# Optimization experiments

Hardware: AMD Instinct MI355X
Metric: run time of the kernel (lower is better)

## Reference

```python
import jax, jax.numpy as jnp
import numpy as np

L, H, C = 2, 8, 128          # layers, heads, hidden_channels
D = C // H                   # head dim
NPAT, NICD, NNDC = 50000, 591, 2042
OUT = 90
E = 250000                   # edges per relation
# edge relations as (src_type, dst_type); node types: 0=patient, 1=icd, 2=ndc
ETYPES = [(0, 1), (1, 0), (0, 2), (2, 0)]


def _seg_softmax(logits, seg, n):
    # softmax over edges grouped by destination node (PyG `softmax`)
    m = jax.ops.segment_max(logits, seg, num_segments=n)
    e = jnp.exp(logits - m[seg])
    s = jax.ops.segment_sum(e, seg, num_segments=n)
    return e / s[seg]


def setup_inputs() -> dict:
    key = jax.random.key(0)
    ks = jax.random.split(key, 24)
    s = 1.0 / np.sqrt(C)
    n = lambda k, shape, sc: jax.random.normal(k, shape, dtype=jnp.float32) * sc
    return {
        "x_patient": n(ks[0], (NPAT, C), 1.0),
        "w_in_patient": n(ks[1], (C, C), s),
        "b_in_patient": jnp.zeros((C,), jnp.float32),
        "emb_icd": n(ks[2], (NICD, C), 0.1),
        "emb_ndc": n(ks[3], (NNDC, C), 0.1),
        "kw": n(ks[4], (L, 3, C, C), s), "kb": jnp.zeros((L, 3, C), jnp.float32),
        "qw": n(ks[5], (L, 3, C, C), s), "qb": jnp.zeros((L, 3, C), jnp.float32),
        "vw": n(ks[6], (L, 3, C, C), s), "vb": jnp.zeros((L, 3, C), jnp.float32),
        "aw": n(ks[7], (L, 3, C, C), s), "ab": jnp.zeros((L, 3, C), jnp.float32),
        "skip": jnp.ones((L, 3), jnp.float32),
        "a_rel": n(ks[8], (L, 4, H, D, D), 1.0 / np.sqrt(D)),
        "m_rel": n(ks[9], (L, 4, H, D, D), 1.0 / np.sqrt(D)),
        "p_rel": jnp.ones((L, 4, H), jnp.float32),
        "w_out": n(ks[10], (C, OUT), s),
        "b_out": jnp.zeros((OUT,), jnp.float32),
        "x_icd": jnp.arange(NICD, dtype=jnp.int32),
        "x_ndc": jnp.arange(NNDC, dtype=jnp.int32),
        "src_pi": jax.random.randint(ks[11], (E,), 0, NPAT, dtype=jnp.int32),
        "dst_pi": jax.random.randint(ks[12], (E,), 0, NICD, dtype=jnp.int32),
        "src_ip": jax.random.randint(ks[13], (E,), 0, NICD, dtype=jnp.int32),
        "dst_ip": jax.random.randint(ks[14], (E,), 0, NPAT, dtype=jnp.int32),
        "src_pn": jax.random.randint(ks[15], (E,), 0, NPAT, dtype=jnp.int32),
        "dst_pn": jax.random.randint(ks[16], (E,), 0, NNDC, dtype=jnp.int32),
        "src_np": jax.random.randint(ks[17], (E,), 0, NNDC, dtype=jnp.int32),
        "dst_np": jax.random.randint(ks[18], (E,), 0, NPAT, dtype=jnp.int32),
    }


def reference(x_patient, w_in_patient, b_in_patient, emb_icd, emb_ndc,
              kw, kb, qw, qb, vw, vb, aw, ab, skip,
              a_rel, m_rel, p_rel, w_out, b_out,
              x_icd, x_ndc,
              src_pi, dst_pi, src_ip, dst_ip, src_pn, dst_pn, src_np, dst_np):
    edges = [(src_pi, dst_pi), (src_ip, dst_ip), (src_pn, dst_pn), (src_np, dst_np)]
    sizes = [NPAT, NICD, NNDC]
    # per-type input projection / embedding + relu
    x = [jax.nn.relu(x_patient @ w_in_patient + b_in_patient),
         jax.nn.relu(emb_icd[x_icd]),
         jax.nn.relu(emb_ndc[x_ndc])]
    scale = 1.0 / np.sqrt(D)
    for l in range(L):
        k = [(x[t] @ kw[l, t] + kb[l, t]).reshape(-1, H, D) for t in range(3)]
        q = [(x[t] @ qw[l, t] + qb[l, t]).reshape(-1, H, D) for t in range(3)]
        v = [(x[t] @ vw[l, t] + vb[l, t]).reshape(-1, H, D) for t in range(3)]
        agg = [jnp.zeros((sizes[t], H, D), x[0].dtype) for t in range(3)]
        for r, (st, dt) in enumerate(ETYPES):
            src, dst = edges[r]
            kr = jnp.einsum('nhd,hde->nhe', k[st], a_rel[l, r])  # relation key transform
            vr = jnp.einsum('nhd,hde->nhe', v[st], m_rel[l, r])  # relation msg transform
            alpha = jnp.sum(q[dt][dst] * kr[src], axis=-1) * p_rel[l, r] * scale  # [E,H]
            alpha = _seg_softmax(alpha, dst, sizes[dt])
            agg[dt] = agg[dt] + jax.ops.segment_sum(vr[src] * alpha[:, :, None], dst, num_segments=sizes[dt])
        new_x = []
        for t in range(3):
            o = jax.nn.gelu(agg[t].reshape(-1, C)) @ aw[l, t] + ab[l, t]
            a = jax.nn.sigmoid(skip[l, t])
            new_x.append(a * o + (1.0 - a) * x[t])  # learned skip (dims match)
        x = new_x
    return jax.nn.sigmoid(x[0] @ w_out + b_out)
```

## Files before the change

### kernel.cpp

```cpp
#include <hip/hip_runtime.h>
#include <math.h>

#define CDIM  128
#define NHEAD 8
#define DHEAD 16
#define NPAT  50000
#define NICD  591
#define NNDC  2042
#define OUTN  90
#define NEDGE 250000
#define NLAYER 2
#define ALC   640

#define OFF0  0
#define OFF1  (NICD)
#define OFF2  (NICD + NPAT)
#define OFF3  (NICD + NPAT + NNDC)
#define NTOT  (NICD + NPAT + NNDC + NPAT)

#define LDP 40
#define CTILE 72
#define LOG2E 1.4426950408889634f

#define NSEG  (2 * NNDC)
#define NAGG  ((NPAT + 3) / 4)

typedef __attribute__((ext_vector_type(8))) short bf16x8;
typedef __attribute__((ext_vector_type(4))) float f32x4;

__device__ __forceinline__ float gelu_tanh(float x) {
    float x3 = x * x * x;
    return 0.5f * x * (1.0f + tanhf(0.7978845608028654f * (x + 0.044715f * x3)));
}
__device__ __forceinline__ float b2f(unsigned short u) {
    union { unsigned int i; float f; } v; v.i = ((unsigned int)u) << 16; return v.f;
}
__device__ __forceinline__ unsigned short f2b(float f) {
    union { float ff; unsigned int i; } v; v.ff = f;
    unsigned int i = v.i;
    return (unsigned short)((i + 0x7FFFu + ((i >> 16) & 1u)) >> 16);
}
__device__ __forceinline__ float2 b2x2(unsigned int u) {
    union { unsigned int i; float f; } lo, hi;
    lo.i = u << 16; hi.i = u & 0xFFFF0000u;
    return make_float2(lo.f, hi.f);
}

// ... 196 lines not shown
        #pragma unroll
        for (int tn = 0; tn < 2; tn++)
        #pragma unroll
        for (int r = 0; r < 4; r++) {
            int row = bm + wr * 32 + tm * 16 + quad * 4 + r;
            int col = bn + wc * 32 + tn * 16 + lm;
            if (row >= M || col >= N) continue;
            float v = acc[tm][tn][r] + (bias ? bias[col] : 0.f);
            if (act == 1) v = fmaxf(v, 0.f);
            else if (act == 2) v = 1.0f / (1.0f + expf(-v));
            ((float*)Cp)[(size_t)row * ldc + col] = v;
        }
    }
}

__global__ __launch_bounds__(256) void wprep_all(
    const float* __restrict__ qw, const float* __restrict__ aw,
    const float* __restrict__ w_in, const float* __restrict__ w_out,
    unsigned short* __restrict__ Wb0, unsigned short* __restrict__ Wb1,
    unsigned short* __restrict__ Wb2, unsigned short* __restrict__ Wtaw,
    unsigned short* __restrict__ Wtin, unsigned short* __restrict__ Wtout)
{
    __shared__ float tile[32][33];
    int z = blockIdx.z;
    const float* s; unsigned short* d; int N = 128;
    if (z < 2)       { s = qw + (size_t)z * 3 * 16384;              d = Wb0 + (size_t)z * 640 * 128; }
    else if (z < 4)  { s = qw + 16384 + (size_t)(z - 2) * 3 * 16384; d = Wb1 + (size_t)(z - 2) * 384 * 128; }
    else if (z < 6)  { s = qw + 2 * 16384 + (size_t)(z - 4) * 3 * 16384; d = Wb2 + (size_t)(z - 4) * 384 * 128; }
    else if (z < 12) { s = aw + (size_t)(z - 6) * 16384;            d = Wtaw + (size_t)(z - 6) * 16384; }
    else if (z == 12){ s = w_in;  d = Wtin; }
    else             { s = w_out; d = Wtout; N = OUTN; }
    int k0 = blockIdx.x * 32, n0 = blockIdx.y * 32;
    int tx = threadIdx.x & 31, ty = threadIdx.x >> 5;
    for (int i = 0; i < 32; i += 8) {
        int k = k0 + ty + i, n = n0 + tx;
        tile[ty + i][tx] = (k < 128 && n < N) ? s[(size_t)k * N + n] : 0.f;
    }
    __syncthreads();
    for (int i = 0; i < 32; i += 8) {
        int n = n0 + ty + i, k = k0 + tx;
        if (n < N && k < 128) d[(size_t)n * 128 + k] = f2b(tile[tx][ty + i]);
    }
}

__global__ __launch_bounds__(256) void wcomp_kernel(
    const float* __restrict__ kw, const float* __restrict__ vw,
    const float* __restrict__ a_rel, const float* __restrict__ m_rel,
    const float* __restrict__ kb, const float* __restrict__ vb,
    unsigned short* __restrict__ Wb0, unsigned short* __restrict__ Wb1,
    unsigned short* __restrict__ Wb2,
    float* __restrict__ bb0, float* __restrict__ bb1, float* __restrict__ bb2)
{
    int s = blockIdx.x;
    int l = s >> 3, j = s & 7;
    int t, isV, r, rowoff, nw;
    unsigned short* Wb; float* bb;
    switch (j) {
      case 0: t=0; isV=0; r=0; Wb=Wb0; bb=bb0; rowoff=128; nw=640; break;
      case 1: t=0; isV=1; r=0; Wb=Wb0; bb=bb0; rowoff=256; nw=640; break;
      case 2: t=0; isV=0; r=2; Wb=Wb0; bb=bb0; rowoff=384; nw=640; break;
      case 3: t=0; isV=1; r=2; Wb=Wb0; bb=bb0; rowoff=512; nw=640; break;
      case 4: t=1; isV=0; r=1; Wb=Wb1; bb=bb1; rowoff=128; nw=384; break;
      case 5: t=1; isV=1; r=1; Wb=Wb1; bb=bb1; rowoff=256; nw=384; break;
      case 6: t=2; isV=0; r=3; Wb=Wb2; bb=bb2; rowoff=128; nw=384; break;
      default:t=2; isV=1; r=3; Wb=Wb2; bb=bb2; rowoff=256; nw=384; break;
    }
    const float* W = (isV ? vw : kw) + (size_t)(l * 3 + t) * 16384;
    const float* A = (isV ? m_rel : a_rel) + (size_t)(l * 4 + r) * 2048;
    const float* B = (isV ? vb : kb) + (size_t)(l * 3 + t) * 128;
    unsigned short* dst = Wb + (size_t)l * nw * 128 + (size_t)rowoff * 128;
    float* bdst = bb + (size_t)l * nw + rowoff;
    int n = threadIdx.x & 127;
    int kh = threadIdx.x >> 7;
    int h = n >> 4, e = n & 15;
    float Ar[16];
    #pragma unroll
    for (int d = 0; d < 16; d++) Ar[d] = A[h * 256 + d * 16 + e];
    for (int k = kh * 64; k < kh * 64 + 64; k++) {
        float acc = 0.f;
        const float* wr = W + (size_t)k * 128 + h * 16;
        #pragma unroll
        for (int d = 0; d < 16; d++) acc += wr[d] * Ar[d];
        dst[(size_t)n * 128 + k] = f2b(acc);
    }
    if (kh == 0) {
        float acc = 0.f;
        const float* br = B + h * 16;
        #pragma unroll
        for (int d = 0; d < 16; d++) acc += br[d] * Ar[d];
        bdst[n] = acc;
    }
}

__global__ void biasq_kernel(const float* __restrict__ qb,
                             float* __restrict__ bb0, float* __restrict__ bb1,
                             float* __restrict__ bb2) {
    int t = blockIdx.x * blockDim.x + threadIdx.x;
    if (t >= 6 * 128) return;
    int g = t >> 7, c = t & 127;
    int l = g / 3, ty = g % 3;
    float v = qb[g * 128 + c];
    if (ty == 0) bb0[l * 640 + c] = v;
    else if (ty == 1) bb1[l * 384 + c] = v;
    else bb2[l * 384 + c] = v;
}

__global__ __launch_bounds__(256) void hist4_kernel(
    const int* __restrict__ d0, const int* __restrict__ d1,
    const int* __restrict__ d2, const int* __restrict__ d3,
    int* __restrict__ deg)
{
    __shared__ int lh[2048];
    int rel = blockIdx.y;
    int t = threadIdx.x;
    const int* dp = (rel == 0) ? d0 : (rel == 1) ? d1 : (rel == 2) ? d2 : d3;
    int off = (rel == 0) ? OFF0 : (rel == 1) ? OFF1 : (rel == 2) ? OFF2 : OFF3;
    if (rel == 1 || rel == 3) {
        for (int e = blockIdx.x * 256 + t; e < NEDGE; e += gridDim.x * 256)
            atomicAdd(&deg[off + dp[e]], 1);
// ... 18 lines not shown
    int b = blockIdx.x, t = threadIdx.x;
    int base = b * 1024 + t * 4;
    int s = 0;
    if (base + 3 < n) {
        int4 v = *(const int4*)(deg + base);
        s = v.x + v.y + v.z + v.w;
    } else {
        for (int i = 0; i < 4; i++) if (base + i < n) s += deg[base + i];
    }
    red[t] = s;
    __syncthreads();
    for (int o = 128; o; o >>= 1) { if (t < o) red[t] += red[t + o]; __syncthreads(); }
    if (t == 0) part[b] = red[0];
}

__global__ __launch_bounds__(128) void scanB_kernel(int* __restrict__ part, int nb)
{
    __shared__ int s[256];
    int t = threadIdx.x;
    for (int i = t; i < nb; i += 128) s[i] = part[i];
    __syncthreads();
    if (t == 0) { int run = 0; for (int i = 0; i < nb; i++) { int v = s[i]; s[i] = run; run += v; } }
    __syncthreads();
    for (int i = t; i < nb; i += 128) part[i] = s[i];
}

__global__ __launch_bounds__(256) void scanC_kernel(
    const int* __restrict__ deg, const int* __restrict__ part,
    int* __restrict__ rp0, int* __restrict__ rp1,
    int* __restrict__ rp2, int* __restrict__ rp3,
    int* __restrict__ cursor, int n)
{
    __shared__ int red[256];
    int b = blockIdx.x, t = threadIdx.x;
    int base = b * 1024 + t * 4;
    int v[4] = {0, 0, 0, 0};
    if (base + 3 < n) {
        int4 q = *(const int4*)(deg + base);
        v[0] = q.x; v[1] = q.y; v[2] = q.z; v[3] = q.w;
    } else {
        for (int i = 0; i < 4; i++) if (base + i < n) v[i] = deg[base + i];
    }
    red[t] = v[0] + v[1] + v[2] + v[3];
    __syncthreads();
    for (int off = 1; off < 256; off <<= 1) {
        int y = (t >= off) ? red[t - off] : 0;
        __syncthreads();
        red[t] += y;
        __syncthreads();
    }
    int run = part[b] + ((t == 0) ? 0 : red[t - 1]);
    for (int i = 0; i < 4; i++) {
        int g = base + i;
        if (g < n) {
            cursor[g] = run;
            int r, loc;
            if      (g < OFF1) { r = 0; loc = g; }
            else if (g < OFF2) { r = 1; loc = g - OFF1; }
            else if (g < OFF3) { r = 2; loc = g - OFF2; }
            else               { r = 3; loc = g - OFF3; }
            int Sl = run - r * NEDGE;
            ((r == 0) ? rp0 : (r == 1) ? rp1 : (r == 2) ? rp2 : rp3)[loc] = Sl;
            run += v[i];
        }
    }
    if (b == 0 && t == 0) {
        rp0[NICD] = NEDGE; rp1[NPAT] = NEDGE; rp2[NNDC] = NEDGE; rp3[NPAT] = NEDGE;
    }
}

__global__ __launch_bounds__(256) void scatter_pack_kernel(
    const int* __restrict__ s0, const int* __restrict__ d0,
    const int* __restrict__ s1, const int* __restrict__ d1,
    const int* __restrict__ s2, const int* __restrict__ d2,
    const int* __restrict__ s3, const int* __restrict__ d3,
    int* __restrict__ cursor, unsigned int* __restrict__ es)
{
    __shared__ int lcnt[2048];
    __shared__ int lbase[2048];
    int rel = blockIdx.y;
    int t = threadIdx.x;
    const int* sp = (rel == 0) ? s0 : (rel == 1) ? s1 : (rel == 2) ? s2 : s3;
    const int* dp = (rel == 0) ? d0 : (rel == 1) ? d1 : (rel == 2) ? d2 : d3;
    int off = (rel == 0) ? OFF0 : (rel == 1) ? OFF1 : (rel == 2) ? OFF2 : OFF3;
    if (rel == 1 || rel == 3) {
        for (int e = blockIdx.x * 256 + t; e < NEDGE; e += gridDim.x * 256) {
            int d = dp[e];
            int p = atomicAdd(&cursor[off + d], 1);
            es[p] = ((unsigned int)sp[e] << 16) | (unsigned int)d;
        }
    } else {
        int nb = (rel == 0) ? NICD : NNDC;
        int per = (NEDGE + gridDim.x - 1) / gridDim.x;
        int e0 = blockIdx.x * per, e1 = min(e0 + per, NEDGE);
        for (int i = t; i < nb; i += 256) lcnt[i] = 0;
        __syncthreads();
        for (int e = e0 + t; e < e1; e += 256) atomicAdd(&lcnt[dp[e]], 1);
        __syncthreads();
        for (int i = t; i < nb; i += 256) {
            int c = lcnt[i];
            lbase[i] = c ? atomicAdd(&cursor[off + i], c) : 0;
            lcnt[i] = 0;
        }
        __syncthreads();
        for (int e = e0 + t; e < e1; e += 256) {
            int d = dp[e];
            int p = lbase[d] + atomicAdd(&lcnt[d], 1);
            es[p] = ((unsigned int)sp[e] << 16) | (unsigned int)d;
        }
    }
}

__global__ void gather_relu2_kernel(
    const float* __restrict__ embA, const int* __restrict__ idxA,
    unsigned short* __restrict__ outA, int nA,
    const float* __restrict__ embB, const int* __restrict__ idxB,
    unsigned short* __restrict__ outB, int nB)
{
    int t = blockIdx.x * blockDim.x + threadIdx.x;
    int totA = nA * CDIM;
    if (t < totA) {
        int r = t >> 7, c = t & 127;
        outA[t] = f2b(fmaxf(embA[(size_t)idxA[r] * CDIM + c], 0.f));
    } else if (t < totA + nB * CDIM) {
        int u = t - totA;
        int r = u >> 7, c = u & 127;
        outB[u] = f2b(fmaxf(embB[(size_t)idxB[r] * CDIM + c], 0.f));
    }
}

__device__ __forceinline__ float dot16_bf(const unsigned short* a,
                                          const unsigned short* b) {
    const uint4* ap = (const uint4*)a;
    const uint4* bp = (const uint4*)b;
    uint4 a0 = ap[0], a1 = ap[1], b0 = bp[0], b1 = bp[1];
    unsigned int au[8] = {a0.x, a0.y, a0.z, a0.w, a1.x, a1.y, a1.z, a1.w};
    unsigned int bu[8] = {b0.x, b0.y, b0.z, b0.w, b1.x, b1.y, b1.z, b1.w};
    float acc = 0.f;
    #pragma unroll
    for (int j = 0; j < 8; j++) {
        float2 x = b2x2(au[j]), y = b2x2(bu[j]);
        acc += x.x * y.x + x.y * y.y;
// ... 134 lines not shown
        for (; i < deg; i += 4) {
            int e0 = sl[i];
            unsigned int u0 = *(const unsigned int*)(vr + (size_t)e0 * ldsrc + 2 * l);
            float w0 = wl[i * NHEAD + hh];
            float2 v0 = b2x2(u0);
            acc0 += w0 * v0.x;
            acc1 += w0 * v0.y;
        }
        p3f[g][l][0] = acc0;
        p3f[g][l][1] = acc1;
        __syncthreads();
        if (t < 128) {
            int c = t;
            float v = p3f[0][c >> 1][c & 1] + p3f[1][c >> 1][c & 1]
                    + p3f[2][c >> 1][c & 1] + p3f[3][c >> 1][c & 1];
            agg[(size_t)n * CDIM + c] = f2b(gelu_tanh(v * sinv[c >> 4]));
        }
    } else {
        float* p3 = (float*)p3f;
        float mx = -1e30f;
        for (int i = j; i < deg; i += 32) {
            int sn = es[r0 + i] >> 16;
            float a = dot16_q(qa, qb, kr + (size_t)sn * ldsrc + h * DHEAD) * ph;
            alpha[(size_t)(r0 + i) * NHEAD + h] = a;
            mx = fmaxf(mx, a);
        }
        mx = fmaxf(mx, __shfl_xor(mx, 8));
        mx = fmaxf(mx, __shfl_xor(mx, 16));
        mx = fmaxf(mx, __shfl_xor(mx, 32));
        if (lane < 8) wred[wv][h] = mx;
        __syncthreads();
// ... 30 lines not shown
            float w2 = alpha[(size_t)(r0 + i + 4) * NHEAD + (c >> 4)];
            float w3 = alpha[(size_t)(r0 + i + 6) * NHEAD + (c >> 4)];
            float v0 = b2f(vr[(size_t)(e0 >> 16) * ldsrc + c]);
            float v1 = b2f(vr[(size_t)(e1 >> 16) * ldsrc + c]);
            float v2 = b2f(vr[(size_t)(e2 >> 16) * ldsrc + c]);
            float v3 = b2f(vr[(size_t)(e3 >> 16) * ldsrc + c]);
            acc += w0 * v0 + w1 * v1 + w2 * v2 + w3 * v3;
        }
        for (; i < deg; i += 2) {
            unsigned int e0 = es[r0 + i];
            float w0 = alpha[(size_t)(r0 + i) * NHEAD + (c >> 4)];
            acc += w0 * b2f(vr[(size_t)(e0 >> 16) * ldsrc + c]);
        }
        p3[t] = acc * hsi;
        __syncthreads();
        if (half == 0) agg[(size_t)n * CDIM + c] = f2b(gelu_tanh(p3[c] + p3[128 + c]));
    }
}

__global__ __launch_bounds__(256) void agg2_kernel(
    const int* __restrict__ rp1, const unsigned int* __restrict__ es1,
    const int* __restrict__ rp3, const unsigned int* __restrict__ es3,
    const unsigned short* __restrict__ q, int ldq,
    const unsigned short* __restrict__ kr1, const unsigned short* __restrict__ vr1, int ld1,
    const unsigned short* __restrict__ kr3, const unsigned short* __restrict__ vr3, int ld3,
    const float* __restrict__ prel1, const float* __restrict__ prel3,
    unsigned short* __restrict__ agg, int nd)
{
    __shared__ float wls[4][128 * NHEAD];
    __shared__ int slo[4][128];
    int wv  = threadIdx.x >> 6;
    int wid = (blockIdx.x * 256 + threadIdx.x) >> 6;
    int lane = threadIdx.x & 63;
    if (wid >= nd) return;
    float* wl = wls[wv];
    int* sl = slo[wv];
    int h = lane & 7, j = lane >> 3;
    int hc = lane >> 3;
    const unsigned short* qbase = q + (size_t)wid * ldq;
    float acc0 = 0.f, acc1 = 0.f;

    int r0a = rp1[wid], degA = rp1[wid + 1] - r0a;
    int r0b = rp3[wid], degB = rp3[wid + 1] - r0b;

    if (degA <= 64 && degB <= 64) {
        const unsigned short* qrow = qbase + h * DHEAD;
        float phA = prel1[h] * 0.25f * LOG2E;
        float phB = prel3[h] * 0.25f * LOG2E;
        int dOfs = (int)(kr3 - kr1);
        float mA = -1e30f, mB = -1e30f;
        for (int i = j; i < degA; i += 8) {
            int sn = es1[r0a + i] >> 16;
            int off = sn * ld1;
            float a = dot16_bf(qrow, kr1 + off + h * DHEAD) * phA;
            wl[i * NHEAD + h] = a;
            if (h == 0) sl[i] = off;
            mA = fmaxf(mA, a);
        }
        for (int i = j; i < degB; i += 8) {
            int sn = es3[r0b + i] >> 16;
            int off = sn * ld3;
            float a = dot16_bf(qrow, kr3 + off + h * DHEAD) * phB;
            wl[(degA + i) * NHEAD + h] = a;
            if (h == 0) sl[degA + i] = dOfs + off;
            mB = fmaxf(mB, a);
        }
        mA = fmaxf(mA, __shfl_xor(mA, 8));   mB = fmaxf(mB, __shfl_xor(mB, 8));
        mA = fmaxf(mA, __shfl_xor(mA, 16));  mB = fmaxf(mB, __shfl_xor(mB, 16));
        mA = fmaxf(mA, __shfl_xor(mA, 32));  mB = fmaxf(mB, __shfl_xor(mB, 32));

        int dtot = degA + degB;
        float sA = 0.f, sB = 0.f;
        for (int i = j; i < dtot; i += 8) {
            bool isA = i < degA;
            float e = exp2f(wl[i * NHEAD + h] - (isA ? mA : mB));
            wl[i * NHEAD + h] = e;
            sA += isA ? e : 0.f;
            sB += isA ? 0.f : e;
        }
        sA += __shfl_xor(sA, 8);   sB += __shfl_xor(sB, 8);
        sA += __shfl_xor(sA, 16);  sB += __shfl_xor(sB, 16);
        sA += __shfl_xor(sA, 32);  sB += __shfl_xor(sB, 32);
        float siA = (sA > 0.f) ? 1.0f / sA : 0.f;
        float siB = (sB > 0.f) ? 1.0f / sB : 0.f;
        for (int i = j; i < dtot; i += 8)
            wl[i * NHEAD + h] *= (i < degA) ? siA : siB;

        int i = 0;
        for (; i + 4 <= dtot; i += 4) {
            int o0 = sl[i + 0], o1 = sl[i + 1], o2 = sl[i + 2], o3 = sl[i + 3];
            unsigned int u0 = *(const unsigned int*)(vr1 + o0 + 2 * lane);
            unsigned int u1 = *(const unsigned int*)(vr1 + o1 + 2 * lane);
            unsigned int u2 = *(const unsigned int*)(vr1 + o2 + 2 * lane);
            unsigned int u3 = *(const unsigned int*)(vr1 + o3 + 2 * lane);
            float w0 = wl[(i + 0) * NHEAD + hc];
            float w1 = wl[(i + 1) * NHEAD + hc];
            float w2 = wl[(i + 2) * NHEAD + hc];
            float w3 = wl[(i + 3) * NHEAD + hc];
            float2 v0 = b2x2(u0), v1 = b2x2(u1), v2 = b2x2(u2), v3 = b2x2(u3);
            acc0 += w0 * v0.x + w1 * v1.x + w2 * v2.x + w3 * v3.x;
            acc1 += w0 * v0.y + w1 * v1.y + w2 * v2.y + w3 * v3.y;
        }
        for (; i < dtot; i++) {
            int o0 = sl[i];
            unsigned int u0 = *(const unsigned int*)(vr1 + o0 + 2 * lane);
            float w0 = wl[i * NHEAD + hc];
            float2 v0 = b2x2(u0);
            acc0 += w0 * v0.x; acc1 += w0 * v0.y;
        }
    } else {
        #pragma unroll
        for (int rr = 0; rr < 2; rr++) {
            const unsigned int* es = rr ? es3 : es1;
            const unsigned short* kr = rr ? kr3 : kr1;
            const unsigned short* vr = rr ? vr3 : vr1;
            int ld = rr ? ld3 : ld1;
            const float* prel = rr ? prel3 : prel1;
            int r0 = rr ? r0b : r0a;
            int deg = rr ? degB : degA;
            if (deg <= 0) continue;
            const unsigned short* qrow = qbase + h * DHEAD;
            float ph = prel[h] * 0.25f * LOG2E;
            bool small = (deg <= 64);

            float m = -1e30f;
// ... 32 lines not shown
            const unsigned short* qrow_hc = qbase + hc * DHEAD;
            for (int i = 0; i < deg; i++) {
                unsigned int sv = es[r0 + i] >> 16;
                unsigned int pv = *(const unsigned int*)(vr + (size_t)sv * ld + 2 * lane);
                float2 v = b2x2(pv);
                float wgt;
                if (small) wgt = wl[i * NHEAD + hc];
                else {
                    float a = dot16_bf(qrow_hc, kr + (size_t)sv * ld + hc * DHEAD) * ph_hc;
                    wgt = exp2f(a - m_hc) * si_hc;
                }
                acc0 += wgt * v.x;
                acc1 += wgt * v.y;
            }
        }
    }
    unsigned int packed = (unsigned int)f2b(gelu_tanh(acc0))
                        | ((unsigned int)f2b(gelu_tanh(acc1)) << 16);
    *(unsigned int*)(agg + (size_t)wid * CDIM + 2 * lane) = packed;
}

extern "C" void kernel_launch(void* const* d_in, const int* in_sizes, int n_in,
                              void* d_out, int out_size, void* d_ws, size_t ws_size,
                              hipStream_t stream)
{
    const float* x_patient = (const float*)d_in[0];
    const float* w_in      = (const float*)d_in[1];
    const float* b_in      = (const float*)d_in[2];
    const float* emb_icd   = (const float*)d_in[3];
    const float* emb_ndc   = (const float*)d_in[4];
    const float* kw        = (const float*)d_in[5];
    const float* kbias     = (const float*)d_in[6];
    const float* qw        = (const float*)d_in[7];
// ... 45 lines not shown
    int* deg    = (int*)alloc((size_t)NTOT * 4);
    int* cursor = (int*)alloc((size_t)NTOT * 4);
    int* part   = (int*)alloc((size_t)256 * 4);
    unsigned short* Wb0   = (unsigned short*)alloc((size_t)2 * 640 * 128 * 2);
    unsigned short* Wb1   = (unsigned short*)alloc((size_t)2 * 384 * 128 * 2);
    unsigned short* Wb2   = (unsigned short*)alloc((size_t)2 * 384 * 128 * 2);
    unsigned short* Wtaw  = (unsigned short*)alloc((size_t)6 * 128 * 128 * 2);
    unsigned short* Wtin  = (unsigned short*)alloc((size_t)128 * 128 * 2);
    unsigned short* Wtout = (unsigned short*)alloc((size_t)OUTN * 128 * 2);
    float* bb0 = (float*)alloc((size_t)2 * 640 * 4);
    float* bb1 = (float*)alloc((size_t)2 * 384 * 4);
    float* bb2 = (float*)alloc((size_t)2 * 384 * 4);
    unsigned int* esRel[4];
    for (int r = 0; r < 4; r++) esRel[r] = esbig + (size_t)r * NEDGE;

    wprep_all<<<dim3(4, 4, 14), 256, 0, stream>>>(qw, aw, w_in, w_out,
        Wb0, Wb1, Wb2, Wtaw, Wtin, Wtout);
    wcomp_kernel<<<16, 256, 0, stream>>>(kw, vw, a_rel, m_rel, kbias, vbias,
        Wb0, Wb1, Wb2, bb0, bb1, bb2);
    biasq_kernel<<<3, 256, 0, stream>>>(qbias, bb0, bb1, bb2);

    {
        const int NB = (NTOT + 1023) / 1024;
        hipMemsetAsync(deg, 0, (size_t)NTOT * 4, stream);
        hist4_kernel<<<dim3(64, 4), 256, 0, stream>>>(
            edst[0], edst[1], edst[2], edst[3], deg);
        scanA_kernel<<<NB, 256, 0, stream>>>(deg, part, NTOT);
        scanB_kernel<<<1, 128, 0, stream>>>(part, NB);
        scanC_kernel<<<NB, 256, 0, stream>>>(deg, part,
            rowptr[0], rowptr[1], rowptr[2], rowptr[3], cursor, NTOT);
        scatter_pack_kernel<<<dim3(64, 4), 256, 0, stream>>>(
            esrc[0], edst[0], esrc[1], edst[1], esrc[2], edst[2], esrc[3], edst[3],
            cursor, esbig);
    }

    {
        int ntile = 2;
        int nwg = ((NPAT + 63) / 64) * ntile;
        gemm_xs<<<dim3(nwg), dim3(256), 0, stream>>>(x_patient, 1, 128, Wtin, b_in,
            xb[0], 0, 128, NPAT, 128, 1, ntile, nullptr, 0, nullptr, 0);
    }
    gather_relu2_kernel<<<((NICD + NNDC) * CDIM + 255) / 256, 256, 0, stream>>>(
        emb_icd, x_icd, xb[1], NICD, emb_ndc, x_ndc, xb[2], NNDC);

    const int ntP0 = 640 / 64, nwgP0 = ((NPAT + 63) / 64) * ntP0;
    const int ntP1 = 384 / 64, nwgP1 = ((NICD + 63) / 64) * ntP1;
    const int ntP2 = 384 / 64, nwgP2 = ((NNDC + 63) / 64) * ntP2;
    const int ntS  = 128 / 64;
    const int nwgS0 = ((NPAT + 63) / 64) * ntS;
    const int nwgS1 = ((NICD + 63) / 64) * ntS;
    const int nwgS2 = ((NNDC + 63) / 64) * ntS;

    for (int l = 0; l < NLAYER; l++) {
        gemm3_kernel<<<dim3(nwgP0 + nwgP1 + nwgP2), dim3(256), 0, stream>>>(
            xb[0], Wb0 + (size_t)l * 640 * 128, bb0 + (size_t)l * 640, P0,
            NPAT, 640, ntP0, nwgP0,
            xb[1], Wb1 + (size_t)l * 384 * 128, bb1 + (size_t)l * 384, P1,
            NICD, 384, ntP1, nwgP0 + nwgP1,
// ... 34 lines not shown
```

Measured before the change: 512.4 us.

## Merge prep launches, fold scan phase, fuse scatter with input GEMM, faster GELU

```diff
diff --git a/kernel.cpp b/kernel.cpp
--- a/kernel.cpp
+++ b/kernel.cpp
@@ -17,6 +17,7 @@
 #define OFF2  (NICD + NPAT)
 #define OFF3  (NICD + NPAT + NNDC)
 #define NTOT  (NICD + NPAT + NNDC + NPAT)
+#define NB_SCAN ((NTOT + 1023) / 1024)
 
 #define LDP 40
 #define CTILE 72
@@ -25,12 +26,24 @@
 #define NSEG  (2 * NNDC)
 #define NAGG  ((NPAT + 3) / 4)
 
+#define PB_W  224
+#define PB_C  (PB_W + 16)
+#define PB_Q  (PB_C + 3)
+#define PB_Z  (PB_Q + NB_SCAN)
+#define PB_G  (PB_Z + (((NICD + NNDC) * CDIM + 255) / 256))
+
+#define SI_SCAT 256
+#define SI_NWG  (((NPAT + 63) / 64) * 2)
+
 typedef __attribute__((ext_vector_type(8))) short bf16x8;
 typedef __attribute__((ext_vector_type(4))) float f32x4;
 
-__device__ __forceinline__ float gelu_tanh(float x) {
+__device__ __forceinline__ float gelu_fast(float x) {
     float x3 = x * x * x;
-    return 0.5f * x * (1.0f + tanhf(0.7978845608028654f * (x + 0.044715f * x3)));
+    float y = 0.7978845608028654f * (x + 0.044715f * x3);
+    float e = exp2f(y * (2.0f * LOG2E));
+    float t = 1.0f - 2.0f * __builtin_amdgcn_rcpf(e + 1.0f);
+    return 0.5f * x * (1.0f + t);
 }
 __device__ __forceinline__ float b2f(unsigned short u) {
     union { unsigned int i; float f; } v; v.i = ((unsigned int)u) << 16; return v.f;
@@ -257,95 +270,113 @@
     }
 }
 
-__global__ __launch_bounds__(256) void wprep_all(
+__global__ __launch_bounds__(256) void prep_all_kernel(
     const float* __restrict__ qw, const float* __restrict__ aw,
     const float* __restrict__ w_in, const float* __restrict__ w_out,
     unsigned short* __restrict__ Wb0, unsigned short* __restrict__ Wb1,
     unsigned short* __restrict__ Wb2, unsigned short* __restrict__ Wtaw,
-    unsigned short* __restrict__ Wtin, unsigned short* __restrict__ Wtout)
-{
-    __shared__ float tile[32][33];
-    int z = blockIdx.z;
-    const float* s; unsigned short* d; int N = 128;
-    if (z < 2)       { s = qw + (size_t)z * 3 * 16384;              d = Wb0 + (size_t)z * 640 * 128; }
-    else if (z < 4)  { s = qw + 16384 + (size_t)(z - 2) * 3 * 16384; d = Wb1 + (size_t)(z - 2) * 384 * 128; }
-    else if (z < 6)  { s = qw + 2 * 16384 + (size_t)(z - 4) * 3 * 16384; d = Wb2 + (size_t)(z - 4) * 384 * 128; }
-    else if (z < 12) { s = aw + (size_t)(z - 6) * 16384;            d = Wtaw + (size_t)(z - 6) * 16384; }
-    else if (z == 12){ s = w_in;  d = Wtin; }
-    else             { s = w_out; d = Wtout; N = OUTN; }
-    int k0 = blockIdx.x * 32, n0 = blockIdx.y * 32;
-    int tx = threadIdx.x & 31, ty = threadIdx.x >> 5;
-    for (int i = 0; i < 32; i += 8) {
-        int k = k0 + ty + i, n = n0 + tx;
-        tile[ty + i][tx] = (k < 128 && n < N) ? s[(size_t)k * N + n] : 0.f;
-    }
-    __syncthreads();
-    for (int i = 0; i < 32; i += 8) {
-        int n = n0 + ty + i, k = k0 + tx;
-        if (n < N && k < 128) d[(size_t)n * 128 + k] = f2b(tile[tx][ty + i]);
-    }
-}
-
-__global__ __launch_bounds__(256) void wcomp_kernel(
+    unsigned short* __restrict__ Wtin, unsigned short* __restrict__ Wtout,
     const float* __restrict__ kw, const float* __restrict__ vw,
     const float* __restrict__ a_rel, const float* __restrict__ m_rel,
     const float* __restrict__ kb, const float* __restrict__ vb,
-    unsigned short* __restrict__ Wb0, unsigned short* __restrict__ Wb1,
-    unsigned short* __restrict__ Wb2,
-    float* __restrict__ bb0, float* __restrict__ bb1, float* __restrict__ bb2)
+    float* __restrict__ bb0, float* __restrict__ bb1, float* __restrict__ bb2,
+    const float* __restrict__ qb,
+    int* __restrict__ deg,
+    const float* __restrict__ emb_icd, const int* __restrict__ x_icd,
+    unsigned short* __restrict__ xb1,
+    const float* __restrict__ emb_ndc, const int* __restrict__ x_ndc,
+    unsigned short* __restrict__ xb2)
 {
-    int s = blockIdx.x;
-    int l = s >> 3, j = s & 7;
-    int t, isV, r, rowoff, nw;
-    unsigned short* Wb; float* bb;
-    switch (j) {
-      case 0: t=0; isV=0; r=0; Wb=Wb0; bb=bb0; rowoff=128; nw=640; break;
-      case 1: t=0; isV=1; r=0; Wb=Wb0; bb=bb0; rowoff=256; nw=640; break;
-      case 2: t=0; isV=0; r=2; Wb=Wb0; bb=bb0; rowoff=384; nw=640; break;
-      case 3: t=0; isV=1; r=2; Wb=Wb0; bb=bb0; rowoff=512; nw=640; break;
-      case 4: t=1; isV=0; r=1; Wb=Wb1; bb=bb1; rowoff=128; nw=384; break;
-      case 5: t=1; isV=1; r=1; Wb=Wb1; bb=bb1; rowoff=256; nw=384; break;
-      case 6: t=2; isV=0; r=3; Wb=Wb2; bb=bb2; rowoff=128; nw=384; break;
-      default:t=2; isV=1; r=3; Wb=Wb2; bb=bb2; rowoff=256; nw=384; break;
-    }
-    const float* W = (isV ? vw : kw) + (size_t)(l * 3 + t) * 16384;
-    const float* A = (isV ? m_rel : a_rel) + (size_t)(l * 4 + r) * 2048;
-    const float* B = (isV ? vb : kb) + (size_t)(l * 3 + t) * 128;
-    unsigned short* dst = Wb + (size_t)l * nw * 128 + (size_t)rowoff * 128;
-    float* bdst = bb + (size_t)l * nw + rowoff;
-    int n = threadIdx.x & 127;
-    int kh = threadIdx.x >> 7;
-    int h = n >> 4, e = n & 15;
-    float Ar[16];
-    #pragma unroll
-    for (int d = 0; d < 16; d++) Ar[d] = A[h * 256 + d * 16 + e];
-    for (int k = kh * 64; k < kh * 64 + 64; k++) {
-        float acc = 0.f;
-        const float* wr = W + (size_t)k * 128 + h * 16;
-        #pragma unroll
-        for (int d = 0; d < 16; d++) acc += wr[d] * Ar[d];
-        dst[(size_t)n * 128 + k] = f2b(acc);
-    }
-    if (kh == 0) {
-        float acc = 0.f;
-        const float* br = B + h * 16;
-        #pragma unroll
-        for (int d = 0; d < 16; d++) acc += br[d] * Ar[d];
-        bdst[n] = acc;
-    }
-}
-
-__global__ void biasq_kernel(const float* __restrict__ qb,
-                             float* __restrict__ bb0, float* __restrict__ bb1,
-                             float* __restrict__ bb2) {
-    int t = blockIdx.x * blockDim.x + threadIdx.x;
-    if (t >= 6 * 128) return;
-    int g = t >> 7, c = t & 127;
-    int l = g / 3, ty = g % 3;
-    float v = qb[g * 128 + c];
-    if (ty == 0) bb0[l * 640 + c] = v;
-    else if (ty == 1) bb1[l * 384 + c] = v;
-    else bb2[l * 384 + c] = v;
+    __shared__ float tile[32][33];
+    int b = blockIdx.x;
+    int tid = threadIdx.x;
+    if (b < PB_W) {
+        int z = b >> 4, rem = b & 15;
+        int by = rem >> 2, bx = rem & 3;
+        const float* s; unsigned short* d; int N = 128;
+        if (z < 2)       { s = qw + (size_t)z * 3 * 16384;               d = Wb0 + (size_t)z * 640 * 128; }
+        else if (z < 4)  { s = qw + 16384 + (size_t)(z - 2) * 3 * 16384; d = Wb1 + (size_t)(z - 2) * 384 * 128; }
+        else if (z < 6)  { s = qw + 2 * 16384 + (size_t)(z - 4) * 3 * 16384; d = Wb2 + (size_t)(z - 4) * 384 * 128; }
+        else if (z < 12) { s = aw + (size_t)(z - 6) * 16384;             d = Wtaw + (size_t)(z - 6) * 16384; }
+        else if (z == 12){ s = w_in;  d = Wtin; }
+        else             { s = w_out; d = Wtout; N = OUTN; }
+        int k0 = bx * 32, n0 = by * 32;
+        int tx = tid & 31, ty = tid >> 5;
+        for (int i = 0; i < 32; i += 8) {
+            int k = k0 + ty + i, n = n0 + tx;
+            tile[ty + i][tx] = (k < 128 && n < N) ? s[(size_t)k * N + n] : 0.f;
+        }
+        __syncthreads();
+        for (int i = 0; i < 32; i += 8) {
+            int n = n0 + ty + i, k = k0 + tx;
+            if (n < N && k < 128) d[(size_t)n * 128 + k] = f2b(tile[tx][ty + i]);
+        }
+    } else if (b < PB_C) {
+        int s = b - PB_W;
+        int l = s >> 3, j = s & 7;
+        int ty, isV, r, rowoff, nw;
+        unsigned short* Wb; float* bb;
+        switch (j) {
+          case 0: ty=0; isV=0; r=0; Wb=Wb0; bb=bb0; rowoff=128; nw=640; break;
+          case 1: ty=0; isV=1; r=0; Wb=Wb0; bb=bb0; rowoff=256; nw=640; break;
+          case 2: ty=0; isV=0; r=2; Wb=Wb0; bb=bb0; rowoff=384; nw=640; break;
+          case 3: ty=0; isV=1; r=2; Wb=Wb0; bb=bb0; rowoff=512; nw=640; break;
+          case 4: ty=1; isV=0; r=1; Wb=Wb1; bb=bb1; rowoff=128; nw=384; break;
+          case 5: ty=1; isV=1; r=1; Wb=Wb1; bb=bb1; rowoff=256; nw=384; break;
+          case 6: ty=2; isV=0; r=3; Wb=Wb2; bb=bb2; rowoff=128; nw=384; break;
+          default:ty=2; isV=1; r=3; Wb=Wb2; bb=bb2; rowoff=256; nw=384; break;
+        }
+        const float* W = (isV ? vw : kw) + (size_t)(l * 3 + ty) * 16384;
+        const float* A = (isV ? m_rel : a_rel) + (size_t)(l * 4 + r) * 2048;
+        const float* B = (isV ? vb : kb) + (size_t)(l * 3 + ty) * 128;
+        unsigned short* dst = Wb + (size_t)l * nw * 128 + (size_t)rowoff * 128;
+        float* bdst = bb + (size_t)l * nw + rowoff;
+        int n = tid & 127;
+        int kh = tid >> 7;
+        int h = n >> 4, e = n & 15;
+        float Ar[16];
+        #pragma unroll
+        for (int d = 0; d < 16; d++) Ar[d] = A[h * 256 + d * 16 + e];
+        for (int k = kh * 64; k < kh * 64 + 64; k++) {
+            float acc = 0.f;
+            const float* wr = W + (size_t)k * 128 + h * 16;
+            #pragma unroll
+            for (int d = 0; d < 16; d++) acc += wr[d] * Ar[d];
+            dst[(size_t)n * 128 + k] = f2b(acc);
+        }
+        if (kh == 0) {
+            float acc = 0.f;
+            const float* br = B + h * 16;
+            #pragma unroll
+            for (int d = 0; d < 16; d++) acc += br[d] * Ar[d];
+            bdst[n] = acc;
+        }
+    } else if (b < PB_Q) {
+        int t = (b - PB_C) * 256 + tid;
+        if (t < 6 * 128) {
+            int g = t >> 7, c = t & 127;
+            int l = g / 3, ty = g % 3;
+            float v = qb[g * 128 + c];
+            if (ty == 0) bb0[l * 640 + c] = v;
+            else if (ty == 1) bb1[l * 384 + c] = v;
+            else bb2[l * 384 + c] = v;
+        }
+    } else if (b < PB_Z) {
+        int base = (b - PB_Q) * 1024 + tid * 4;
+        if (base + 3 < NTOT) *(int4*)(deg + base) = make_int4(0, 0, 0, 0);
+        else for (int i = 0; i < 4; i++) if (base + i < NTOT) deg[base + i] = 0;
+    } else {
+        int t = (b - PB_Z) * 256 + tid;
+        int totA = NICD * CDIM;
+        if (t < totA) {
+            int r = t >> 7, c = t & 127;
+            xb1[t] = f2b(fmaxf(emb_icd[(size_t)x_icd[r] * CDIM + c], 0.f));
+        } else if (t < totA + NNDC * CDIM) {
+            int u = t - totA;
+            int r = u >> 7, c = u & 127;
+            xb2[u] = f2b(fmaxf(emb_ndc[(size_t)x_ndc[r] * CDIM + c], 0.f));
+        }
+    }
 }
 
 __global__ __launch_bounds__(256) void hist4_kernel(
@@ -394,25 +425,21 @@
     if (t == 0) part[b] = red[0];
 }
 
-__global__ __launch_bounds__(128) void scanB_kernel(int* __restrict__ part, int nb)
-{
-    __shared__ int s[256];
-    int t = threadIdx.x;
-    for (int i = t; i < nb; i += 128) s[i] = part[i];
-    __syncthreads();
-    if (t == 0) { int run = 0; for (int i = 0; i < nb; i++) { int v = s[i]; s[i] = run; run += v; } }
-    __syncthreads();
-    for (int i = t; i < nb; i += 128) part[i] = s[i];
-}
-
-__global__ __launch_bounds__(256) void scanC_kernel(
+__global__ __launch_bounds__(256) void scanC2_kernel(
     const int* __restrict__ deg, const int* __restrict__ part,
     int* __restrict__ rp0, int* __restrict__ rp1,
     int* __restrict__ rp2, int* __restrict__ rp3,
     int* __restrict__ cursor, int n)
 {
     __shared__ int red[256];
+    __shared__ int pre[128];
     int b = blockIdx.x, t = threadIdx.x;
+    if (t < 128) pre[t] = (t < b) ? part[t] : 0;
+    __syncthreads();
+    for (int o = 64; o; o >>= 1) { if (t < o) pre[t] += pre[t + o]; __syncthreads(); }
+    int pbase = pre[0];
+    __syncthreads();
+
     int base = b * 1024 + t * 4;
     int v[4] = {0, 0, 0, 0};
     if (base + 3 < n) {
@@ -429,7 +456,7 @@
         red[t] += y;
         __syncthreads();
     }
-    int run = part[b] + ((t == 0) ? 0 : red[t - 1]);
+    int run = pbase + ((t == 0) ? 0 : red[t - 1]);
     for (int i = 0; i < 4; i++) {
         int g = base + i;
         if (g < n) {
@@ -449,63 +476,120 @@
     }
 }
 
-__global__ __launch_bounds__(256) void scatter_pack_kernel(
+__global__ __launch_bounds__(256) void scat_in_kernel(
     const int* __restrict__ s0, const int* __restrict__ d0,
     const int* __restrict__ s1, const int* __restrict__ d1,
     const int* __restrict__ s2, const int* __restrict__ d2,
     const int* __restrict__ s3, const int* __restrict__ d3,
-    int* __restrict__ cursor, unsigned int* __restrict__ es)
+    int* __restrict__ cursor, unsigned int* __restrict__ es,
+    const float* __restrict__ Axp, const unsigned short* __restrict__ Wtin,
+    const float* __restrict__ b_in, unsigned short* __restrict__ xb0)
 {
-    __shared__ int lcnt[2048];
-    __shared__ int lbase[2048];
-    int rel = blockIdx.y;
+    __shared__ __align__(16) char smem[19456];
+    int b = blockIdx.x;
     int t = threadIdx.x;
-    const int* sp = (rel == 0) ? s0 : (rel == 1) ? s1 : (rel == 2) ? s2 : s3;
-    const int* dp = (rel == 0) ? d0 : (rel == 1) ? d1 : (rel == 2) ? d2 : d3;
-    int off = (rel == 0) ? OFF0 : (rel == 1) ? OFF1 : (rel == 2) ? OFF2 : OFF3;
-    if (rel == 1 || rel == 3) {
-        for (int e = blockIdx.x * 256 + t; e < NEDGE; e += gridDim.x * 256) {
-            int d = dp[e];
-            int p = atomicAdd(&cursor[off + d], 1);
-            es[p] = ((unsigned int)sp[e] << 16) | (unsigned int)d;
+    if (b < SI_SCAT) {
+        int* lcnt = (int*)smem;
+        int* lbase = lcnt + 2048;
+        int rel = b >> 6;
+        int bx = b & 63;
+        const int* sp = (rel == 0) ? s0 : (rel == 1) ? s1 : (rel == 2) ? s2 : s3;
+        const int* dp = (rel == 0) ? d0 : (rel == 1) ? d1 : (rel == 2) ? d2 : d3;
+        int off = (rel == 0) ? OFF0 : (rel == 1) ? OFF1 : (rel == 2) ? OFF2 : OFF3;
+        if (rel == 1 || rel == 3) {
+            for (int e = bx * 256 + t; e < NEDGE; e += 64 * 256) {
+                int d = dp[e];
+                int p = atomicAdd(&cursor[off + d], 1);
+                es[p] = ((unsigned int)sp[e] << 16) | (unsigned int)d;
+            }
+        } else {
+            int nb = (rel == 0) ? NICD : NNDC;
+            int per = (NEDGE + 63) / 64;
+            int e0 = bx * per, e1 = min(e0 + per, NEDGE);
+            for (int i = t; i < nb; i += 256) lcnt[i] = 0;
+            __syncthreads();
+            for (int e = e0 + t; e < e1; e += 256) atomicAdd(&lcnt[dp[e]], 1);
+            __syncthreads();
+            for (int i = t; i < nb; i += 256) {
+                int c = lcnt[i];
+                lbase[i] = c ? atomicAdd(&cursor[off + i], c) : 0;
+                lcnt[i] = 0;
+            }
+            __syncthreads();
+            for (int e = e0 + t; e < e1; e += 256) {
+                int d = dp[e];
+                int p = lbase[d] + atomicAdd(&lcnt[d], 1);
+                es[p] = ((unsigned int)sp[e] << 16) | (unsigned int)d;
+            }
         }
     } else {
-        int nb = (rel == 0) ? NICD : NNDC;
-        int per = (NEDGE + gridDim.x - 1) / gridDim.x;
-        int e0 = blockIdx.x * per, e1 = min(e0 + per, NEDGE);
-        for (int i = t; i < nb; i += 256) lcnt[i] = 0;
-        __syncthreads();
-        for (int e = e0 + t; e < e1; e += 256) atomicAdd(&lcnt[dp[e]], 1);
-        __syncthreads();
-        for (int i = t; i < nb; i += 256) {
-            int c = lcnt[i];
-            lbase[i] = c ? atomicAdd(&cursor[off + i], c) : 0;
-            lcnt[i] = 0;
-        }
-        __syncthreads();
-        for (int e = e0 + t; e < e1; e += 256) {
-            int d = dp[e];
-            int p = lbase[d] + atomicAdd(&lcnt[d], 1);
-            es[p] = ((unsigned int)sp[e] << 16) | (unsigned int)d;
-        }
-    }
-}
-
-__global__ void gather_relu2_kernel(
-    const float* __restrict__ embA, const int* __restrict__ idxA,
-    unsigned short* __restrict__ outA, int nA,
-    const float* __restrict__ embB, const int* __restrict__ idxB,
-    unsigned short* __restrict__ outB, int nB)
-{
-    int t = blockIdx.x * blockDim.x + threadIdx.x;
-    int totA = nA * CDIM;
-    if (t < totA) {
-        int r = t >> 7, c = t & 127;
-        outA[t] = f2b(fmaxf(embA[(size_t)idxA[r] * CDIM + c], 0.f));
-    } else if (t < totA + nB * CDIM) {
-        int u = t - totA;
-        int r = u >> 7, c = u & 127;
-        outB[u] = f2b(fmaxf(embB[(size_t)idxB[r] * CDIM + c], 0.f));
+        unsigned short* Al = (unsigned short*)smem;
+        unsigned short* Bl = Al + 64 * LDP;
+        unsigned short* Cst = Bl + 64 * LDP;
+        int u = b - SI_SCAT;
+        int nwg = SI_NWG;
+        int qq = nwg >> 3, rr = nwg & 7;
+        int xcd = u & 7, idx = u >> 3;
+        int wgid = (xcd < rr ? xcd * (qq + 1) : rr * (qq + 1) + (xcd - rr) * qq) + idx;
+        int bm = (wgid >> 1) * 64, bn = (wgid & 1) * 64;
+
+        int lane = t & 63, w = t >> 6;
+        int wr = w >> 1, wc = w & 1;
+        int quad = lane >> 4, lm = lane & 15;
+        f32x4 acc[2][2] = {};
+        const int srow = t >> 2;
+        const int skq  = (t & 3) * 8;
+
+        for (int k0 = 0; k0 < 128; k0 += 32) {
+            {
+                int row = bm + srow;
+                float f[8] = {0.f,0.f,0.f,0.f,0.f,0.f,0.f,0.f};
+                if (row < NPAT) {
+                    const float4* ap = (const float4*)(Axp + (size_t)row * 128 + k0 + skq);
+                    float4 u0 = ap[0], u1 = ap[1];
+                    f[0]=u0.x; f[1]=u0.y; f[2]=u0.z; f[3]=u0.w;
+                    f[4]=u1.x; f[5]=u1.y; f[6]=u1.z; f[7]=u1.w;
+                }
+                unsigned short v[8];
+                for (int i = 0; i < 8; i++) v[i] = f2b(f[i]);
+                *(uint4*)&Al[srow * LDP + skq] = *(uint4*)v;
+            }
+            {
+                int n = bn + srow;
+                *(uint4*)&Bl[srow * LDP + skq] = *(const uint4*)(Wtin + (size_t)n * 128 + k0 + skq);
+            }
+            __syncthreads();
+            bf16x8 af[2], bfr[2];
+            #pragma unroll
+            for (int i = 0; i < 2; i++) {
+                af[i]  = *(const bf16x8*)&Al[(wr * 32 + i * 16 + lm) * LDP + quad * 8];
+                bfr[i] = *(const bf16x8*)&Bl[(wc * 32 + i * 16 + lm) * LDP + quad * 8];
+            }
+            acc[0][0] = __builtin_amdgcn_mfma_f32_16x16x32_bf16(af[0], bfr[0], acc[0][0], 0, 0, 0);
+            acc[0][1] = __builtin_amdgcn_mfma_f32_16x16x32_bf16(af[0], bfr[1], acc[0][1], 0, 0, 0);
+            acc[1][0] = __builtin_amdgcn_mfma_f32_16x16x32_bf16(af[1], bfr[0], acc[1][0], 0, 0, 0);
+            acc[1][1] = __builtin_amdgcn_mfma_f32_16x16x32_bf16(af[1], bfr[1], acc[1][1], 0, 0, 0);
+            __syncthreads();
+        }
+        #pragma unroll
+        for (int tm = 0; tm < 2; tm++)
+        #pragma unroll
+        for (int tn = 0; tn < 2; tn++)
+        #pragma unroll
+        for (int r = 0; r < 4; r++) {
+            int lrow = wr * 32 + tm * 16 + quad * 4 + r;
+            int lcol = wc * 32 + tn * 16 + lm;
+            float v = acc[tm][tn][r] + b_in[bn + lcol];
+            v = fmaxf(v, 0.f);
+            Cst[lrow * CTILE + lcol] = f2b(v);
+        }
+        __syncthreads();
+        int row = t >> 2, seg = (t & 3) * 16;
+        if (bm + row < NPAT) {
+            unsigned short* dst = xb0 + (size_t)(bm + row) * 128 + bn + seg;
+            *(uint4*)dst       = *(const uint4*)&Cst[row * CTILE + seg];
+            *(uint4*)(dst + 8) = *(const uint4*)&Cst[row * CTILE + seg + 8];
+        }
     }
 }
 
@@ -670,7 +754,7 @@
             int c = t;
             float v = p3f[0][c >> 1][c & 1] + p3f[1][c >> 1][c & 1]
                     + p3f[2][c >> 1][c & 1] + p3f[3][c >> 1][c & 1];
-            agg[(size_t)n * CDIM + c] = f2b(gelu_tanh(v * sinv[c >> 4]));
+            agg[(size_t)n * CDIM + c] = f2b(gelu_fast(v * sinv[c >> 4]));
         }
     } else {
         float* p3 = (float*)p3f;
@@ -731,7 +815,7 @@
         }
         p3[t] = acc * hsi;
         __syncthreads();
-        if (half == 0) agg[(size_t)n * CDIM + c] = f2b(gelu_tanh(p3[c] + p3[128 + c]));
+        if (half == 0) agg[(size_t)n * CDIM + c] = f2b(gelu_fast(p3[c] + p3[128 + c]));
     }
 }
 
@@ -755,13 +839,14 @@
     int h = lane & 7, j = lane >> 3;
     int hc = lane >> 3;
     const unsigned short* qbase = q + (size_t)wid * ldq;
-    float acc0 = 0.f, acc1 = 0.f;
 
     int r0a = rp1[wid], degA = rp1[wid + 1] - r0a;
     int r0b = rp3[wid], degB = rp3[wid + 1] - r0b;
 
+    float o0, o1;
     if (degA <= 64 && degB <= 64) {
         const unsigned short* qrow = qbase + h * DHEAD;
+        uint4 qa = ((const uint4*)qrow)[0], qb = ((const uint4*)qrow)[1];
         float phA = prel1[h] * 0.25f * LOG2E;
         float phB = prel3[h] * 0.25f * LOG2E;
         int dOfs = (int)(kr3 - kr1);
@@ -769,7 +854,7 @@
         for (int i = j; i < degA; i += 8) {
             int sn = es1[r0a + i] >> 16;
             int off = sn * ld1;
-            float a = dot16_bf(qrow, kr1 + off + h * DHEAD) * phA;
+            float a = dot16_q(qa, qb, kr1 + off + h * DHEAD) * phA;
             wl[i * NHEAD + h] = a;
             if (h == 0) sl[i] = off;
             mA = fmaxf(mA, a);
@@ -777,7 +862,7 @@
         for (int i = j; i < degB; i += 8) {
             int sn = es3[r0b + i] >> 16;
             int off = sn * ld3;
-            float a = dot16_bf(qrow, kr3 + off + h * DHEAD) * phB;
+            float a = dot16_q(qa, qb, kr3 + off + h * DHEAD) * phB;
             wl[(degA + i) * NHEAD + h] = a;
             if (h == 0) sl[degA + i] = dOfs + off;
             mB = fmaxf(mB, a);
@@ -800,32 +885,57 @@
         sA += __shfl_xor(sA, 32);  sB += __shfl_xor(sB, 32);
         float siA = (sA > 0.f) ? 1.0f / sA : 0.f;
         float siB = (sB > 0.f) ? 1.0f / sB : 0.f;
-        for (int i = j; i < dtot; i += 8)
-            wl[i * NHEAD + h] *= (i < degA) ? siA : siB;
-
+        float siAh = __shfl(siA, hc);
+        float siBh = __shfl(siB, hc);
+
+        float accA0 = 0.f, accA1 = 0.f, accB0 = 0.f, accB1 = 0.f;
         int i = 0;
-        for (; i + 4 <= dtot; i += 4) {
-            int o0 = sl[i + 0], o1 = sl[i + 1], o2 = sl[i + 2], o3 = sl[i + 3];
-            unsigned int u0 = *(const unsigned int*)(vr1 + o0 + 2 * lane);
-            unsigned int u1 = *(const unsigned int*)(vr1 + o1 + 2 * lane);
-            unsigned int u2 = *(const unsigned int*)(vr1 + o2 + 2 * lane);
-            unsigned int u3 = *(const unsigned int*)(vr1 + o3 + 2 * lane);
+        for (; i + 4 <= degA; i += 4) {
+            int oo0 = sl[i + 0], oo1 = sl[i + 1], oo2 = sl[i + 2], oo3 = sl[i + 3];
+            unsigned int u0 = *(const unsigned int*)(vr1 + oo0 + 2 * lane);
+            unsigned int u1 = *(const unsigned int*)(vr1 + oo1 + 2 * lane);
+            unsigned int u2 = *(const unsigned int*)(vr1 + oo2 + 2 * lane);
+            unsigned int u3 = *(const unsigned int*)(vr1 + oo3 + 2 * lane);
             float w0 = wl[(i + 0) * NHEAD + hc];
             float w1 = wl[(i + 1) * NHEAD + hc];
             float w2 = wl[(i + 2) * NHEAD + hc];
             float w3 = wl[(i + 3) * NHEAD + hc];
             float2 v0 = b2x2(u0), v1 = b2x2(u1), v2 = b2x2(u2), v3 = b2x2(u3);
-            acc0 += w0 * v0.x + w1 * v1.x + w2 * v2.x + w3 * v3.x;
-            acc1 += w0 * v0.y + w1 * v1.y + w2 * v2.y + w3 * v3.y;
-        }
-        for (; i < dtot; i++) {
-            int o0 = sl[i];
-            unsigned int u0 = *(const unsigned int*)(vr1 + o0 + 2 * lane);
+            accA0 += w0 * v0.x + w1 * v1.x + w2 * v2.x + w3 * v3.x;
+            accA1 += w0 * v0.y + w1 * v1.y + w2 * v2.y + w3 * v3.y;
+        }
+        for (; i < degA; i++) {
+            int oo = sl[i];
+            unsigned int u0 = *(const unsigned int*)(vr1 + oo + 2 * lane);
             float w0 = wl[i * NHEAD + hc];
             float2 v0 = b2x2(u0);
-            acc0 += w0 * v0.x; acc1 += w0 * v0.y;
-        }
+            accA0 += w0 * v0.x; accA1 += w0 * v0.y;
+        }
+        for (; i + 4 <= dtot; i += 4) {
+            int oo0 = sl[i + 0], oo1 = sl[i + 1], oo2 = sl[i + 2], oo3 = sl[i + 3];
+            unsigned int u0 = *(const unsigned int*)(vr1 + oo0 + 2 * lane);
+            unsigned int u1 = *(const unsigned int*)(vr1 + oo1 + 2 * lane);
+            unsigned int u2 = *(const unsigned int*)(vr1 + oo2 + 2 * lane);
+            unsigned int u3 = *(const unsigned int*)(vr1 + oo3 + 2 * lane);
+            float w0 = wl[(i + 0) * NHEAD + hc];
+            float w1 = wl[(i + 1) * NHEAD + hc];
+            float w2 = wl[(i + 2) * NHEAD + hc];
+            float w3 = wl[(i + 3) * NHEAD + hc];
+            float2 v0 = b2x2(u0), v1 = b2x2(u1), v2 = b2x2(u2), v3 = b2x2(u3);
+            accB0 += w0 * v0.x + w1 * v1.x + w2 * v2.x + w3 * v3.x;
+            accB1 += w0 * v0.y + w1 * v1.y + w2 * v2.y + w3 * v3.y;
+        }
+        for (; i < dtot; i++) {
+            int oo = sl[i];
+            unsigned int u0 = *(const unsigned int*)(vr1 + oo + 2 * lane);
+            float w0 = wl[i * NHEAD + hc];
+            float2 v0 = b2x2(u0);
+            accB0 += w0 * v0.x; accB1 += w0 * v0.y;
+        }
+        o0 = accA0 * siAh + accB0 * siBh;
+        o1 = accA1 * siAh + accB1 * siBh;
     } else {
+        float acc0 = 0.f, acc1 = 0.f;
         #pragma unroll
         for (int rr = 0; rr < 2; rr++) {
             const unsigned int* es = rr ? es3 : es1;
@@ -888,9 +998,10 @@
                 acc1 += wgt * v.y;
             }
         }
-    }
-    unsigned int packed = (unsigned int)f2b(gelu_tanh(acc0))
-                        | ((unsigned int)f2b(gelu_tanh(acc1)) << 16);
+        o0 = acc0; o1 = acc1;
+    }
+    unsigned int packed = (unsigned int)f2b(gelu_fast(o0))
+                        | ((unsigned int)f2b(gelu_fast(o1)) << 16);
     *(unsigned int*)(agg + (size_t)wid * CDIM + 2 * lane) = packed;
 }
 
@@ -966,34 +1077,20 @@
     unsigned int* esRel[4];
     for (int r = 0; r < 4; r++) esRel[r] = esbig + (size_t)r * NEDGE;
 
-    wprep_all<<<dim3(4, 4, 14), 256, 0, stream>>>(qw, aw, w_in, w_out,
-        Wb0, Wb1, Wb2, Wtaw, Wtin, Wtout);
-    wcomp_kernel<<<16, 256, 0, stream>>>(kw, vw, a_rel, m_rel, kbias, vbias,
-        Wb0, Wb1, Wb2, bb0, bb1, bb2);
-    biasq_kernel<<<3, 256, 0, stream>>>(qbias, bb0, bb1, bb2);
-
-    {
-        const int NB = (NTOT + 1023) / 1024;
-        hipMemsetAsync(deg, 0, (size_t)NTOT * 4, stream);
-        hist4_kernel<<<dim3(64, 4), 256, 0, stream>>>(
-            edst[0], edst[1], edst[2], edst[3], deg);
-        scanA_kernel<<<NB, 256, 0, stream>>>(deg, part, NTOT);
-        scanB_kernel<<<1, 128, 0, stream>>>(part, NB);
-        scanC_kernel<<<NB, 256, 0, stream>>>(deg, part,
-            rowptr[0], rowptr[1], rowptr[2], rowptr[3], cursor, NTOT);
-        scatter_pack_kernel<<<dim3(64, 4), 256, 0, stream>>>(
-            esrc[0], edst[0], esrc[1], edst[1], esrc[2], edst[2], esrc[3], edst[3],
-            cursor, esbig);
-    }
-
-    {
-        int ntile = 2;
-        int nwg = ((NPAT + 63) / 64) * ntile;
-        gemm_xs<<<dim3(nwg), dim3(256), 0, stream>>>(x_patient, 1, 128, Wtin, b_in,
-            xb[0], 0, 128, NPAT, 128, 1, ntile, nullptr, 0, nullptr, 0);
-    }
-    gather_relu2_kernel<<<((NICD + NNDC) * CDIM + 255) / 256, 256, 0, stream>>>(
-        emb_icd, x_icd, xb[1], NICD, emb_ndc, x_ndc, xb[2], NNDC);
+    prep_all_kernel<<<dim3(PB_G), dim3(256), 0, stream>>>(
+        qw, aw, w_in, w_out, Wb0, Wb1, Wb2, Wtaw, Wtin, Wtout,
+        kw, vw, a_rel, m_rel, kbias, vbias, bb0, bb1, bb2, qbias,
+        deg, emb_icd, x_icd, xb[1], emb_ndc, x_ndc, xb[2]);
+
+    hist4_kernel<<<dim3(64, 4), 256, 0, stream>>>(
+        edst[0], edst[1], edst[2], edst[3], deg);
+    scanA_kernel<<<NB_SCAN, 256, 0, stream>>>(deg, part, NTOT);
+    scanC2_kernel<<<NB_SCAN, 256, 0, stream>>>(deg, part,
+        rowptr[0], rowptr[1], rowptr[2], rowptr[3], cursor, NTOT);
+
+    scat_in_kernel<<<dim3(SI_SCAT + SI_NWG), 256, 0, stream>>>(
+        esrc[0], edst[0], esrc[1], edst[1], esrc[2], edst[2], esrc[3], edst[3],
+        cursor, esbig, x_patient, Wtin, b_in, xb[0]);
 
     const int ntP0 = 640 / 64, nwgP0 = ((NPAT + 63) / 64) * ntP0;
     const int ntP1 = 384 / 64, nwgP1 = ((NICD + 63) / 64) * ntP1;
```

Result: faster. 488.7 us (-4.6%).
